# Performance work log

Measured on AMD Instinct MI355X. Metric: run time of the kernel, lower is better.

The kernel has to match this reference:

```python
import jax, jax.numpy as jnp
import numpy as np

N = 250000   # atoms
E = 500000   # directed bond edges
B = 10000    # molecules
IN = 39      # atom feature dim (in_channels)
H = 128      # hidden_channels
ED = 10      # edge_dim
NUM_TIMESTEPS = 2


def setup_inputs() -> dict:
    key = jax.random.key(0)
    ks = iter(jax.random.split(key, 40))
    p = lambda shape: jax.random.normal(next(ks), shape, dtype=jnp.float32) * 0.05
    inp = {}
    inp["x"] = jax.random.normal(next(ks), (N, IN), dtype=jnp.float32)
    inp["edge_attr"] = jax.random.normal(next(ks), (E, ED), dtype=jnp.float32)
    # lin1
    inp["W_lin1"] = p((H, IN)); inp["b_lin1"] = p((H,))
    # GATEConv
    inp["gate_W1"] = p((H, H + ED)); inp["gate_W2"] = p((H, H))
    inp["gate_att_l"] = p((H,)); inp["gate_att_r"] = p((H,)); inp["gate_bias"] = p((H,))
    # GRUCell after GATEConv
    inp["gru1_Wih"] = p((3 * H, H)); inp["gru1_Whh"] = p((3 * H, H))
    inp["gru1_bih"] = p((3 * H,)); inp["gru1_bhh"] = p((3 * H,))
    # atom GATConv (num_layers-1 == 1)
    inp["conv_W"] = p((H, H)); inp["conv_att_src"] = p((H,)); inp["conv_att_dst"] = p((H,)); inp["conv_bias"] = p((H,))
    inp["gru2_Wih"] = p((3 * H, H)); inp["gru2_Whh"] = p((3 * H, H))
    inp["gru2_bih"] = p((3 * H,)); inp["gru2_bhh"] = p((3 * H,))
    # mol GATConv (bipartite atoms -> molecules, shared lin)
    inp["mol_W"] = p((H, H)); inp["mol_att_src"] = p((H,)); inp["mol_att_dst"] = p((H,)); inp["mol_bias"] = p((H,))
    inp["grum_Wih"] = p((3 * H, H)); inp["grum_Whh"] = p((3 * H, H))
    inp["grum_bih"] = p((3 * H,)); inp["grum_bhh"] = p((3 * H,))
    # lin2 + head
    inp["W_lin2"] = p((H, H)); inp["b_lin2"] = p((H,))
    inp["W_head"] = p((1, H)); inp["b_head"] = p((1,))
    inp["edge_index"] = jax.random.randint(next(ks), (2, E), 0, N, dtype=jnp.int32)
    inp["batch"] = jnp.sort(jax.random.randint(next(ks), (N,), 0, B, dtype=jnp.int32))
    return inp


def _gru(xg, hg, Wih, Whh, bih, bhh):
    # torch.nn.GRUCell semantics
    gi = xg @ Wih.T + bih
    gh = hg @ Whh.T + bhh
    ir, iz, inn = jnp.split(gi, 3, axis=-1)
    hr, hz, hn = jnp.split(gh, 3, axis=-1)
    r = jax.nn.sigmoid(ir + hr)
    z = jax.nn.sigmoid(iz + hz)
    n = jnp.tanh(inn + r * hn)
    return (1.0 - z) * n + z * hg


def _seg_softmax(logits, seg, num):
    # PyG softmax over target-index segments (stable, +1e-16 denom)
    m = jax.ops.segment_max(logits, seg, num_segments=num)
    e = jnp.exp(logits - m[seg])
    s = jax.ops.segment_sum(e, seg, num_segments=num)
    return e / (s[seg] + 1e-16)


def reference(x, edge_attr, W_lin1, b_lin1, gate_W1, gate_W2, gate_att_l, gate_att_r, gate_bias,
              gru1_Wih, gru1_Whh, gru1_bih, gru1_bhh,
              conv_W, conv_att_src, conv_att_dst, conv_bias,
              gru2_Wih, gru2_Whh, gru2_bih, gru2_bhh,
              mol_W, mol_att_src, mol_att_dst, mol_bias,
              grum_Wih, grum_Whh, grum_bih, grum_bhh,
              W_lin2, b_lin2, W_head, b_head,
              edge_index, batch):
    lrelu = lambda v: jax.nn.leaky_relu(v, 0.01)
    src, dst = edge_index[0], edge_index[1]  # (j, i): messages flow j -> i
    # initial atom embedding
    x = lrelu(x @ W_lin1.T + b_lin1)
    # ---- GATEConv (edge-attr-aware attention, aggr='add') ----
    xj = x[src]                                                   # [E, H]
    he = lrelu(jnp.concatenate([xj, edge_attr], axis=-1) @ gate_W1.T)
    alpha = lrelu(he @ gate_att_l + x[dst] @ gate_att_r)          # [E]
    alpha = _seg_softmax(alpha, dst, N)
    h = jax.ops.segment_sum((xj @ gate_W2.T) * alpha[:, None], dst, num_segments=N) + gate_bias
    h = jax.nn.elu(h)
    x = jax.nn.relu(_gru(h, x, gru1_Wih, gru1_Whh, gru1_bih, gru1_bhh))
    # ---- atom GATConv (heads=1, neg_slope=0.01, no self loops) ----
    xl = x @ conv_W.T
    a = lrelu((xl * conv_att_src).sum(-1)[src] + (xl * conv_att_dst).sum(-1)[dst])
    a = _seg_softmax(a, dst, N)
    h = jax.ops.segment_sum(xl[src] * a[:, None], dst, num_segments=N) + conv_bias
    h = jax.nn.relu(h)
    x = jax.nn.relu(_gru(h, x, gru2_Wih, gru2_Whh, gru2_bih, gru2_bhh))
    # ---- attentive graph readout: bipartite GAT atoms -> molecules ----
    out = jax.nn.relu(jax.ops.segment_sum(x, batch, num_segments=B))  # [B, H]
    for _ in range(NUM_TIMESTEPS):
        xs = x @ mol_W.T                                          # src transform [N, H]
        od = out @ mol_W.T                                        # dst transform [B, H]
        a = lrelu((xs * mol_att_src).sum(-1) + ((od * mol_att_dst).sum(-1))[batch])
        a = _seg_softmax(a, batch, B)
        h = jax.ops.segment_sum(xs * a[:, None], batch, num_segments=B) + mol_bias
        h = jax.nn.elu(h)
        out = jax.nn.relu(_gru(h, out, grum_Wih, grum_Whh, grum_bih, grum_bhh))
    out = out @ W_lin2.T + b_lin2
    out = out @ W_head.T + b_head                                 # [B, 1]
    return out.squeeze(-1)                                        # [B]
```

## Files before the change

### kernel.cpp

```cpp
#include <hip/hip_runtime.h>
#include <hip/hip_bf16.h>
#include <type_traits>

typedef __hip_bfloat16 bf16;

constexpr int N_  = 250000;
constexpr int E_  = 500000;
constexpr int B_  = 10000;
constexpr int H_  = 128;

typedef short s8v __attribute__((ext_vector_type(8)));
typedef float f4v __attribute__((ext_vector_type(4)));

__device__ __forceinline__ float b2f(bf16 v){ return __bfloat162float(v); }
__device__ __forceinline__ bf16  f2b(float v){ return __float2bfloat16(v); }
__device__ __forceinline__ float lrelu_f(float v){ return v > 0.f ? v : 0.01f*v; }
__device__ __forceinline__ float sigmoid_f(float x){ return __builtin_amdgcn_rcpf(1.f+__expf(-x)); }
__device__ __forceinline__ float tanh_f(float x){ return 1.f - 2.f*__builtin_amdgcn_rcpf(__expf(2.f*x)+1.f); }
__device__ __forceinline__ float elu_f(float v){ return v > 0.f ? v : __expf(v)-1.f; }
__device__ __forceinline__ unsigned f2b_bits(float f){
  bf16 h=__float2bfloat16(f); unsigned short s; __builtin_memcpy(&s,&h,2); return (unsigned)s;
}
__device__ __forceinline__ void unp8(uint4 v, float* o){
  o[0]=__uint_as_float(v.x<<16); o[1]=__uint_as_float(v.x&0xffff0000u);
  o[2]=__uint_as_float(v.y<<16); o[3]=__uint_as_float(v.y&0xffff0000u);
  o[4]=__uint_as_float(v.z<<16); o[5]=__uint_as_float(v.z&0xffff0000u);
  o[6]=__uint_as_float(v.w<<16); o[7]=__uint_as_float(v.w&0xffff0000u);
}

struct W2B { const float* s; bf16* d; int rows, ld, ow, cw; };
struct W2B9 { W2B seg[9]; };
__global__ void w2ball_k(W2B9 p){
  W2B g=p.seg[blockIdx.y];
  int i=blockIdx.x*256+threadIdx.x;
  if (i>=g.rows*g.ow) return;
  int r=i/g.ow, k=i-r*g.ow;
  g.d[i] = f2b(k<g.cw ? g.s[(size_t)r*g.ld+k] : 0.f);
}

__global__ __launch_bounds__(256) void lin1_mfma_k(const float* __restrict__ X0, const bf16* __restrict__ Wb,
                            const float* __restrict__ bias, const float* __restrict__ dvec,
                            bf16* __restrict__ Y, float* __restrict__ dout, int M){
  __shared__ __align__(16) bf16 sx[64][72];
  __shared__ float sdot[4][64];
  int wv=threadIdx.x>>6, lane=threadIdx.x&63;
  int n=lane&15, q=lane>>4;
  int c0=wv*32;
  s8v wB[2][2];
  #pragma unroll
  for (int ct=0;ct<2;ct++)
    #pragma unroll
    for (int kk=0;kk<2;kk++)
      wB[ct][kk]=*(const s8v*)(Wb+(size_t)(c0+ct*16+n)*64+kk*32+q*8);
  float bb[2];
  #pragma unroll
  for (int ct=0;ct<2;ct++) bb[ct]=bias[c0+ct*16+n];
  float va[2]={dvec[c0+n], dvec[c0+16+n]};
  for (int i=threadIdx.x;i<64*25;i+=256){ int r=i/25,k=39+(i-(i/25)*25); sx[r][k]=f2b(0.f); }
  for (long r0=(long)blockIdx.x*64; r0<M; r0+=(long)gridDim.x*64){
    __syncthreads();
    for (int f=threadIdx.x; f<64*39; f+=256){
      int r=f/39, k=f-(f/39)*39; long row=r0+r;
      sx[r][k]= f2b(row<M ? X0[row*39+k] : 0.f);
    }
    __syncthreads();
    s8v a[4][2];
    #pragma unroll
    for (int rt=0;rt<4;rt++)
      #pragma unroll
      for (int kk=0;kk<2;kk++)
        a[rt][kk]=*(const s8v*)&sx[rt*16+n][kk*32+q*8];
    f4v acc[4][2];
    #pragma unroll
    for (int rt=0;rt<4;rt++)
      #pragma unroll
      for (int ct=0;ct<2;ct++) acc[rt][ct]=(f4v){0.f,0.f,0.f,0.f};
    #pragma unroll
    for (int kk=0;kk<2;kk++)
      #pragma unroll
      for (int rt=0;rt<4;rt++)
        #pragma unroll
        for (int ct=0;ct<2;ct++)
          acc[rt][ct]=__builtin_amdgcn_mfma_f32_16x16x32_bf16(a[rt][kk],wB[ct][kk],acc[rt][ct],0,0,0);
    #pragma unroll
    for (int rt=0;rt<4;rt++){
      #pragma unroll
      for (int rg=0;rg<4;rg++){
        float y0=lrelu_f(acc[rt][0][rg]+bb[0]);
        float y1=lrelu_f(acc[rt][1][rg]+bb[1]);
        long row=r0+rt*16+q*4+rg;
        if (row<M){
          Y[row*128+c0+n]   =f2b(y0);
          Y[row*128+c0+16+n]=f2b(y1);
        }
        float pa=y0*va[0]+y1*va[1];
        #pragma unroll
        for (int o=1;o<16;o<<=1) pa+=__shfl_xor(pa,o);
        if (n==0) sdot[wv][rt*16+q*4+rg]=pa;
      }
    }
    __syncthreads();
    if (threadIdx.x<64){
      long row=r0+threadIdx.x;
      if (row<M) dout[row]=sdot[0][threadIdx.x]+sdot[1][threadIdx.x]+sdot[2][threadIdx.x]+sdot[3][threadIdx.x];
    }
  }
}

template<int ACT,int NDOT>
__global__ __launch_bounds__(256) void lin_mfma_k(const bf16* __restrict__ X, const bf16* __restrict__ Wb,
                            const float* __restrict__ bias, bf16* __restrict__ Y,
                            const float* __restrict__ v1, const float* __restrict__ v2,
                            float* __restrict__ d1, float* __restrict__ d2, int M){
  __shared__ float sdot[2][4][64];
  int wv=threadIdx.x>>6, lane=threadIdx.x&63;
  int n=lane&15, q=lane>>4;
  int c0=wv*32;
  s8v wB[2][4];
  #pragma unroll
  for (int ct=0;ct<2;ct++)
    #pragma unroll
    for (int kk=0;kk<4;kk++)
      wB[ct][kk]=*(const s8v*)(Wb+(size_t)(c0+ct*16+n)*128+kk*32+q*8);
  float bb[2];
  #pragma unroll
  for (int ct=0;ct<2;ct++) bb[ct]=bias? bias[c0+ct*16+n]:0.f;
  float va[2][2];
  if constexpr (NDOT>=1){ va[0][0]=v1[c0+n]; va[0][1]=v1[c0+16+n]; }
  if constexpr (NDOT>=2){ va[1][0]=v2[c0+n]; va[1][1]=v2[c0+16+n]; }
  for (long r0=(long)blockIdx.x*64; r0<M; r0+=(long)gridDim.x*64){
    s8v a[4][4];
    #pragma unroll
    for (int rt=0;rt<4;rt++){
      long row=r0+rt*16+n; if (row>=M) row=M-1;
      #pragma unroll
      for (int kk=0;kk<4;kk++) a[rt][kk]=*(const s8v*)(X+row*128+kk*32+q*8);
    }
    f4v acc[4][2];
    #pragma unroll
    for (int rt=0;rt<4;rt++)
      #pragma unroll
      for (int ct=0;ct<2;ct++) acc[rt][ct]=(f4v){0.f,0.f,0.f,0.f};
    #pragma unroll
    for (int kk=0;kk<4;kk++)
      #pragma unroll
      for (int rt=0;rt<4;rt++)
        #pragma unroll
        for (int ct=0;ct<2;ct++)
          acc[rt][ct]=__builtin_amdgcn_mfma_f32_16x16x32_bf16(a[rt][kk],wB[ct][kk],acc[rt][ct],0,0,0);
    #pragma unroll
    for (int rt=0;rt<4;rt++){
      #pragma unroll
      for (int rg=0;rg<4;rg++){
        float y0=acc[rt][0][rg]+bb[0];
        float y1=acc[rt][1][rg]+bb[1];
        if (ACT==2){ y0=elu_f(y0); y1=elu_f(y1); }
        long row=r0+rt*16+q*4+rg;
        if (row<M){
          Y[row*128+c0+n]   =f2b(y0);
          Y[row*128+c0+16+n]=f2b(y1);
        }
        if constexpr (NDOT>=1){
          float pa=y0*va[0][0]+y1*va[0][1];
          float pb=0.f;
          if constexpr (NDOT>=2) pb=y0*va[1][0]+y1*va[1][1];
          #pragma unroll
          for (int o=1;o<16;o<<=1){
            pa+=__shfl_xor(pa,o);
            if constexpr (NDOT>=2) pb+=__shfl_xor(pb,o);
          }
          if (n==0){
            sdot[0][wv][rt*16+q*4+rg]=pa;
            if constexpr (NDOT>=2) sdot[1][wv][rt*16+q*4+rg]=pb;
          }
        }
      }
    }
    if constexpr (NDOT>=1){
      __syncthreads();
      if (threadIdx.x<64){
        long row=r0+threadIdx.x;
        if (row<M){
          d1[row]=sdot[0][0][threadIdx.x]+sdot[0][1][threadIdx.x]+sdot[0][2][threadIdx.x]+sdot[0][3][threadIdx.x];
          if constexpr (NDOT>=2)
            d2[row]=sdot[1][0][threadIdx.x]+sdot[1][1][threadIdx.x]+sdot[1][2][threadIdx.x]+sdot[1][3][threadIdx.x];
        }
      }
      __syncthreads();
    }
  }
}

__global__ __launch_bounds__(512,1) void gru_mfma_k(const bf16* __restrict__ A, const bf16* __restrict__ X,
                            const bf16* __restrict__ Wih, const bf16* __restrict__ Whh,
                            const float* __restrict__ bih, const float* __restrict__ bhh,
                            bf16* __restrict__ dest, int M){
  __shared__ __align__(16) bf16 sA[2][32][136];
  __shared__ __align__(16) bf16 sX[2][32][136];
  int wv=threadIdx.x>>6, lane=threadIdx.x&63;
  int n=lane&15, q=lane>>4;
  int c0=wv*16;
  s8v wI[3][4], wH[3][4];
  #pragma unroll
  for (int g=0;g<3;g++)
    #pragma unroll
    for (int kk=0;kk<4;kk++){
      size_t off=((size_t)(g*128+c0+n))*128+kk*32+q*8;
      wI[g][kk]=*(const s8v*)(Wih+off);
      wH[g][kk]=*(const s8v*)(Whh+off);
    }
  int col=c0+n;
  float br =bih[col]+bhh[col];
  float bz =bih[128+col]+bhh[128+col];
  float bni=bih[256+col], bnh=bhh[256+col];

  int srow=wv*4+q;
  int schunk=n;
  long step=(long)gridDim.x*32;
  long r0=(long)blockIdx.x*32;
  int buf=0;
  {
    long rowg=r0+srow; if (rowg>=M) rowg=M-1;
    uint4 va=*(const uint4*)(A+rowg*128+schunk*8);
    uint4 vx=*(const uint4*)(X+rowg*128+schunk*8);
    *(uint4*)&sA[0][srow][schunk*8]=va;
    *(uint4*)&sX[0][srow][schunk*8]=vx;
  }
  __syncthreads();
  for (; r0<M; r0+=step){
    long rn=r0+step;
    uint4 va, vx; bool pre = rn<M;
    if (pre){
      long rowg=rn+srow; if (rowg>=M) rowg=M-1;
      va=*(const uint4*)(A+rowg*128+schunk*8);
      vx=*(const uint4*)(X+rowg*128+schunk*8);
    }
    f4v acc[6][2];
    #pragma unroll
    for (int g=0;g<6;g++)
      #pragma unroll
      for (int rt=0;rt<2;rt++) acc[g][rt]=(f4v){0.f,0.f,0.f,0.f};
    #pragma unroll
    for (int kk=0;kk<4;kk++){
      s8v aA[2], aX[2];
      #pragma unroll
      for (int rt=0;rt<2;rt++){
        aA[rt]=*(const s8v*)&sA[buf][rt*16+n][(kk*4+q)*8];
        aX[rt]=*(const s8v*)&sX[buf][rt*16+n][(kk*4+q)*8];
      }
      #pragma unroll
      for (int g=0;g<3;g++)
        #pragma unroll
        for (int rt=0;rt<2;rt++){
          acc[g  ][rt]=__builtin_amdgcn_mfma_f32_16x16x32_bf16(aA[rt],wI[g][kk],acc[g  ][rt],0,0,0);
          acc[3+g][rt]=__builtin_amdgcn_mfma_f32_16x16x32_bf16(aX[rt],wH[g][kk],acc[3+g][rt],0,0,0);
        }
    }
    float xv[2][4];
    #pragma unroll
    for (int rt=0;rt<2;rt++)
      #pragma unroll
      for (int rg=0;rg<4;rg++)
        xv[rt][rg]=b2f(sX[buf][rt*16+q*4+rg][col]);
    #pragma unroll
    for (int rt=0;rt<2;rt++){
      #pragma unroll
      for (int rg=0;rg<4;rg++){
        long row=r0+rt*16+q*4+rg;
        if (row<M){
          float rgate=sigmoid_f(acc[0][rt][rg]+acc[3][rt][rg]+br);
          float zgate=sigmoid_f(acc[1][rt][rg]+acc[4][rt][rg]+bz);
          float nn=tanh_f(acc[2][rt][rg]+bni + rgate*(acc[5][rt][rg]+bnh));
          float o=(1.f-zgate)*nn + zgate*xv[rt][rg];
          dest[row*128+col]=f2b(fmaxf(o,0.f));
        }
      }
    }
    if (pre){
      *(uint4*)&sA[buf^1][srow][schunk*8]=va;
      *(uint4*)&sX[buf^1][srow][schunk*8]=vx;
    }
    __syncthreads();
    buf^=1;
  }
}

__global__ __launch_bounds__(256) void gru_scalar_k(const float* __restrict__ A, const float* __restrict__ X,
                            const float* __restrict__ Wih, const float* __restrict__ Whh,
                            const float* __restrict__ bih, const float* __restrict__ bhh,
                            float* __restrict__ dest, int M){
  __shared__ unsigned sW[6][32*66];
  __shared__ float sA[8][132], sX[8][132];
  __shared__ float sbi[3][32], sbh[3][32];
  int c0 = blockIdx.y*32;
  for (int i=threadIdx.x; i<6*32*64; i+=256){
    int m=i>>11, r=i&2047, c=r>>6, k2=r&63;
    const float* base = (m<3)? Wih : Whh;
    int g = (m<3)? m : m-3;
    const float* wp = base + ((size_t)(g*128 + c0 + c))*128 + 2*k2;
    sW[m][c*66 + k2] = f2b_bits(wp[0]) | (f2b_bits(wp[1])<<16);
  }
  if (threadIdx.x < 96){
    int g=threadIdx.x>>5, c=threadIdx.x&31;
    sbi[g][c]=bih[g*128+c0+c]; sbh[g][c]=bhh[g*128+c0+c];
  }
  __syncthreads();
  int sub=threadIdx.x>>5, c=threadIdx.x&31;
  for (long r0=(long)blockIdx.x*8; r0<M; r0+=(long)gridDim.x*8){
    __syncthreads();
    for (int i=threadIdx.x;i<8*16;i+=256){
      int rr=i>>4, q=i&15; long row=r0+rr;
      if (row<M){
        *(float4*)&sA[rr][q*8]   = *(const float4*)(A+row*128+q*8);
        *(float4*)&sA[rr][q*8+4] = *(const float4*)(A+row*128+q*8+4);
        *(float4*)&sX[rr][q*8]   = *(const float4*)(X+row*128+q*8);
        *(float4*)&sX[rr][q*8+4] = *(const float4*)(X+row*128+q*8+4);
      } else {
        float4 z=make_float4(0,0,0,0);
        *(float4*)&sA[rr][q*8]=z; *(float4*)&sA[rr][q*8+4]=z;
        *(float4*)&sX[rr][q*8]=z; *(float4*)&sX[rr][q*8+4]=z;
      }
    }
    __syncthreads();
    long row=r0+sub;
    if (row<M){
      const unsigned* wri=&sW[0][c*66]; const unsigned* wzi=&sW[1][c*66]; const unsigned* wni=&sW[2][c*66];
      const unsigned* wrh=&sW[3][c*66]; const unsigned* wzh=&sW[4][c*66]; const unsigned* wnh=&sW[5][c*66];
      const float2* xa=(const float2*)sA[sub]; const float2* xb=(const float2*)sX[sub];
      float ari=0,azi=0,ani=0,arh=0,azh=0,anh=0;
      #pragma unroll 8
      for (int k2=0;k2<64;k2++){
        float2 av=xa[k2], bv=xb[k2];
        unsigned u;
        u=wri[k2]; ari += av.x*__uint_as_float(u<<16) + av.y*__uint_as_float(u&0xffff0000u);
        u=wzi[k2]; azi += av.x*__uint_as_float(u<<16) + av.y*__uint_as_float(u&0xffff0000u);
        u=wni[k2]; ani += av.x*__uint_as_float(u<<16) + av.y*__uint_as_float(u&0xffff0000u);
        u=wrh[k2]; arh += bv.x*__uint_as_float(u<<16) + bv.y*__uint_as_float(u&0xffff0000u);
        u=wzh[k2]; azh += bv.x*__uint_as_float(u<<16) + bv.y*__uint_as_float(u&0xffff0000u);
        u=wnh[k2]; anh += bv.x*__uint_as_float(u<<16) + bv.y*__uint_as_float(u&0xffff0000u);
      }
      float rg = sigmoid_f(ari+arh+sbi[0][c]+sbh[0][c]);
      float zg = sigmoid_f(azi+azh+sbi[1][c]+sbh[1][c]);
      float nn = tanh_f(ani+sbi[2][c] + rg*(anh+sbh[2][c]));
      float xv = sX[sub][c0+c];
      float o  = (1.f-zg)*nn + zg*xv;
      dest[row*128+c0+c] = fmaxf(o,0.f);
    }
  }
}

__global__ __launch_bounds__(256) void gate_edge_logits_k(const bf16* __restrict__ u, const float* __restrict__ ea,
                                   const float* __restrict__ gW1, const float* __restrict__ att_l,
                                   const float* __restrict__ ddst, const int* __restrict__ src,
                                   const int* __restrict__ dst, const int* __restrict__ epos,
                                   float* __restrict__ elog, int E){
  int wv=threadIdx.x>>6, lane=threadIdx.x&63;
  int t=lane&31;
  float w[10][4];
  #pragma unroll
  for (int k=0;k<10;k++)
    #pragma unroll
    for (int j=0;j<4;j++)
      w[k][j]=gW1[(size_t)(t*4+j)*138 + 128 + k];
  float al[4];
  #pragma unroll
  for (int j=0;j<4;j++) al[j]=att_l[t*4+j];

  long stride=(long)gridDim.x*8;
  long e=(long)blockIdx.x*8 + wv*2 + (lane>>5);
  if (e>=E) return;
  int sj=src[e];
  uint2 uv=*(const uint2*)(u+(size_t)sj*128+t*4);
  const float2* er=(const float2*)(ea+(size_t)e*10);
  float2 c0=er[0],c1=er[1],c2=er[2],c3=er[3],c4=er[4];
  float dv=ddst[dst[e]];
  int ep=epos[e];
  while (true){
    long en=e+stride; bool has=en<E;
    uint2 uvn=make_uint2(0,0);
    float2 d0={0,0},d1={0,0},d2={0,0},d3={0,0},d4={0,0};
    float dvn=0.f; int epn=0;
    if (has){
      int sjn=src[en];
      uvn=*(const uint2*)(u+(size_t)sjn*128+t*4);
      const float2* ern=(const float2*)(ea+(size_t)en*10);
      d0=ern[0];d1=ern[1];d2=ern[2];d3=ern[3];d4=ern[4];
      dvn=ddst[dst[en]];
      epn=epos[en];
    }
    float uf[4];
    uf[0]=__uint_as_float(uv.x<<16); uf[1]=__uint_as_float(uv.x&0xffff0000u);
    uf[2]=__uint_as_float(uv.y<<16); uf[3]=__uint_as_float(uv.y&0xffff0000u);
    float acc=0.f;
    #pragma unroll
    for (int j=0;j<4;j++){
      float v=uf[j];
      v+=c0.x*w[0][j]; v+=c0.y*w[1][j];
      v+=c1.x*w[2][j]; v+=c1.y*w[3][j];
      v+=c2.x*w[4][j]; v+=c2.y*w[5][j];
      v+=c3.x*w[6][j]; v+=c3.y*w[7][j];
      v+=c4.x*w[8][j]; v+=c4.y*w[9][j];
      acc+=lrelu_f(v)*al[j];
    }
    #pragma unroll
    for (int o=16;o;o>>=1) acc+=__shfl_xor(acc,o);
    if (t==0) elog[ep]=lrelu_f(acc+dv);
    if (!has) break;
    e=en; uv=uvn; c0=d0;c1=d1;c2=d2;c3=d3;c4=d4; dv=dvn; ep=epn;
  }
}

template<int ACT>
__global__ void node_gather_k(const float* __restrict__ elog, const int* __restrict__ srcp,
                              const int* __restrict__ ptr, const bf16* __restrict__ V,
                              const float* __restrict__ bias, bf16* __restrict__ S, int M){
  int wv=threadIdx.x>>6, lane=threadIdx.x&63;
  int g=lane>>3, t=lane&7;
  int node=blockIdx.x*32 + wv*8 + g;
  if (node>=M) return;
  int p0=ptr[node], p1=ptr[node+1];
  float m=-INFINITY;
  for (int p=p0+t;p<p1;p+=8) m=fmaxf(m,elog[p]);
  #pragma unroll
  for (int o=4;o;o>>=1) m=fmaxf(m,__shfl_xor(m,o));
  float ssum=0.f;
  float acc[16]={0,0,0,0,0,0,0,0,0,0,0,0,0,0,0,0};
  if (p0<p1){
    float lg=elog[p0];
    const uint4* vp=(const uint4*)(V+(size_t)srcp[p0]*128+t*16);
    uint4 va=vp[0], vb=vp[1];
    for (int p=p0+1;p<p1;p++){
      float lgn=elog[p];
      const uint4* vpn=(const uint4*)(V+(size_t)srcp[p]*128+t*16);
      uint4 van=vpn[0], vbn=vpn[1];
      float e=__expf(lg-m); ssum+=e;
      float xf[8]; unp8(va,xf);
      #pragma unroll
      for (int j=0;j<8;j++) acc[j]+=e*xf[j];
      unp8(vb,xf);
      #pragma unroll
      for (int j=0;j<8;j++) acc[8+j]+=e*xf[j];
      lg=lgn; va=van; vb=vbn;
    }
    float e=__expf(lg-m); ssum+=e;
    float xf[8]; unp8(va,xf);
    #pragma unroll
    for (int j=0;j<8;j++) acc[j]+=e*xf[j];
    unp8(vb,xf);
    #pragma unroll
    for (int j=0;j<8;j++) acc[8+j]+=e*xf[j];
  }
  float inv=1.f/(ssum+1e-16f);
  #pragma unroll
  for (int j=0;j<16;j++) acc[j]*=inv;
  if (ACT==1){
    #pragma unroll
    for (int j=0;j<16;j++) acc[j]=fmaxf(acc[j]+bias[t*16+j],0.f);
  }
  uint4 o1,o2;
  o1.x=f2b_bits(acc[0])|(f2b_bits(acc[1])<<16);
  o1.y=f2b_bits(acc[2])|(f2b_bits(acc[3])<<16);
  o1.z=f2b_bits(acc[4])|(f2b_bits(acc[5])<<16);
  o1.w=f2b_bits(acc[6])|(f2b_bits(acc[7])<<16);
  o2.x=f2b_bits(acc[8])|(f2b_bits(acc[9])<<16);
  o2.y=f2b_bits(acc[10])|(f2b_bits(acc[11])<<16);
  o2.z=f2b_bits(acc[12])|(f2b_bits(acc[13])<<16);
  o2.w=f2b_bits(acc[14])|(f2b_bits(acc[15])<<16);
  *(uint4*)(S+(size_t)node*128+t*16)=o1;
  *(uint4*)(S+(size_t)node*128+t*16+8)=o2;
}

__global__ __launch_bounds__(256) void conv_gather_k(const float* __restrict__ dsrc, const float* __restrict__ ddst,
    const int* __restrict__ ptr, const int* __restrict__ srcp,
    const bf16* __restrict__ V, const float* __restrict__ bias, bf16* __restrict__ S, int M){
  int wv=threadIdx.x>>6, lane=threadIdx.x&63;
  int g=lane>>3, t=lane&7;
  int node=blockIdx.x*32 + wv*8 + g;
  if (node>=M) return;
  int p0=ptr[node], p1=ptr[node+1];
  float dvn=ddst[node];
  float m=-INFINITY, s=0.f;
  float acc[16]={0,0,0,0,0,0,0,0,0,0,0,0,0,0,0,0};
  if (p0<p1){
    int sj=srcp[p0];
    float ls=dsrc[sj];
    const uint4* vp=(const uint4*)(V+(size_t)sj*128+t*16);
    uint4 va=vp[0], vb=vp[1];
    for (int p=p0+1;p<p1;p++){
      int sjn=srcp[p];
      float lsn=dsrc[sjn];
      const uint4* vpn=(const uint4*)(V+(size_t)sjn*128+t*16);
      uint4 van=vpn[0], vbn=vpn[1];
      float l=lrelu_f(ls+dvn);
      float mn=fmaxf(m,l), sc=__expf(m-mn), ee=__expf(l-mn);
      float xf[8]; unp8(va,xf);
      s=s*sc+ee;
      #pragma unroll
      for (int j=0;j<8;j++) acc[j]=acc[j]*sc+ee*xf[j];
      unp8(vb,xf);
      #pragma unroll
      for (int j=0;j<8;j++) acc[8+j]=acc[8+j]*sc+ee*xf[j];
      m=mn; ls=lsn; va=van; vb=vbn;
    }
    float l=lrelu_f(ls+dvn);
    float mn=fmaxf(m,l), sc=__expf(m-mn), ee=__expf(l-mn);
    float xf[8]; unp8(va,xf);
    s=s*sc+ee;
    #pragma unroll
    for (int j=0;j<8;j++) acc[j]=acc[j]*sc+ee*xf[j];
    unp8(vb,xf);
    #pragma unroll
    for (int j=0;j<8;j++) acc[8+j]=acc[8+j]*sc+ee*xf[j];
  }
  float inv=1.f/(s+1e-16f);
  float r[16];
  #pragma unroll
  for (int j=0;j<16;j++) r[j]=fmaxf(acc[j]*inv+bias[t*16+j],0.f);
  uint4 o1,o2;
  o1.x=f2b_bits(r[0])|(f2b_bits(r[1])<<16);
  o1.y=f2b_bits(r[2])|(f2b_bits(r[3])<<16);
  o1.z=f2b_bits(r[4])|(f2b_bits(r[5])<<16);
  o1.w=f2b_bits(r[6])|(f2b_bits(r[7])<<16);
  o2.x=f2b_bits(r[8])|(f2b_bits(r[9])<<16);
  o2.y=f2b_bits(r[10])|(f2b_bits(r[11])<<16);
  o2.z=f2b_bits(r[12])|(f2b_bits(r[13])<<16);
  o2.w=f2b_bits(r[14])|(f2b_bits(r[15])<<16);
  *(uint4*)(S+(size_t)node*128+t*16)=o1;
  *(uint4*)(S+(size_t)node*128+t*16+8)=o2;
}

__global__ void mol_ptr_k(const int* __restrict__ batch, int* __restrict__ mptr, int n, int Bn){
  int b=blockIdx.x*256+threadIdx.x; if (b>Bn) return;
  if (b==Bn){ mptr[Bn]=n; return; }
  int lo=0, hi=n;
  while (lo<hi){ int mid=(lo+hi)>>1; if (batch[mid]<b) lo=mid+1; else hi=mid; }
  mptr[b]=lo;
}

__global__ void mol_sum_k(const bf16* __restrict__ x, const int* __restrict__ mptr,
                          float* __restrict__ out, int Bn){
  int wv=threadIdx.x>>6, lane=threadIdx.x&63;
  int b=blockIdx.x*4+wv; if (b>=Bn) return;
  int p0=mptr[b], p1=mptr[b+1];
  float a0=0.f,a1=0.f;
  for (int i=p0;i<p1;i++){ a0+=b2f(x[(size_t)i*128+lane]); a1+=b2f(x[(size_t)i*128+64+lane]); }
  out[(size_t)b*128+lane]=fmaxf(a0,0.f); out[(size_t)b*128+64+lane]=fmaxf(a1,0.f);
}

__global__ void fold_att_k(const float* __restrict__ W, const float* __restrict__ att,
                           float* __restrict__ wdd){
  int k=threadIdx.x; float a=0.f;
  for (int c=0;c<128;c++) a+=att[c]*W[(size_t)c*128+k];
  wdd[k]=a;
}

__global__ __launch_bounds__(256) void mol_fused_k(const float* __restrict__ dsrc, const int* __restrict__ mptr,
    const bf16* __restrict__ xs, const float* __restrict__ wdd, const float* __restrict__ outc,
    const float* __restrict__ bias, float* __restrict__ hb, int Bn){
  int wv=threadIdx.x>>6, lane=threadIdx.x&63;
  long b=(long)blockIdx.x*4+wv; if (b>=Bn) return;
  int p0=mptr[b], p1=mptr[b+1];
  float dd=outc[(size_t)b*128+lane]*wdd[lane]+outc[(size_t)b*128+64+lane]*wdd[64+lane];
  #pragma unroll
  for (int o=32;o;o>>=1) dd+=__shfl_xor(dd,o);
  float m=-INFINITY, s=0.f, a0=0.f, a1=0.f;
  for (int i=p0;i<p1;i++){
    float a=lrelu_f(dsrc[i]+dd);
    float x0=b2f(xs[(size_t)i*128+lane]), x1=b2f(xs[(size_t)i*128+64+lane]);
    float mn=fmaxf(m,a), sc=__expf(m-mn), ee=__expf(a-mn);
    s=s*sc+ee; a0=a0*sc+ee*x0; a1=a1*sc+ee*x1; m=mn;
  }
  float inv=1.f/(s+1e-16f);
  hb[(size_t)b*128+lane]=elu_f(a0*inv+bias[lane]);
  hb[(size_t)b*128+64+lane]=elu_f(a1*inv+bias[64+lane]);
}

__global__ void fold_head_k(const float* __restrict__ W2, const float* __restrict__ b2,
                            const float* __restrict__ Wh, const float* __restrict__ bh,
                            float* __restrict__ v){
  __shared__ float sred[128];
  int k=threadIdx.x;
  float a=0.f;
  for (int c=0;c<128;c++) a+=Wh[c]*W2[(size_t)c*128+k];
  v[k]=a;
  sred[k]=b2[k]*Wh[k]; __syncthreads();
  for (int o=64;o;o>>=1){ if (k<o) sred[k]+=sred[k+o]; __syncthreads(); }
  if (k==0) v[128]=sred[0]+bh[0];
}

__global__ void head_dot_k(const float* __restrict__ out, const float* __restrict__ v,
                           float* __restrict__ y, int M){
  __shared__ float sv[129];
  if (threadIdx.x<129) sv[threadIdx.x]=v[threadIdx.x];
  __syncthreads();
  int wv=threadIdx.x>>6, lane=threadIdx.x&63;
  long row=(long)blockIdx.x*4+wv;
  if (row>=M) return;
  float a=out[row*128+lane]*sv[lane]+out[row*128+64+lane]*sv[64+lane];
  #pragma unroll
  for (int o=32;o;o>>=1) a+=__shfl_xor(a,o);
  if (!lane) y[row]=a+sv[128];
}

__global__ void zero_i32_k(int* p, int n){ int i=blockIdx.x*256+threadIdx.x; if (i<n) p[i]=0; }
__global__ void hist_k(const int* __restrict__ dst, int* __restrict__ deg, int n){
  int e=blockIdx.x*256+threadIdx.x; if (e<n) atomicAdd(&deg[dst[e]],1);
}
__global__ void scan1_k(const int* __restrict__ deg, int* __restrict__ ptr,
                        int* __restrict__ part, int n){
  __shared__ int sd[256];
  int base=blockIdx.x*1024, tid=threadIdx.x;
  int v[4]; int ssum=0;
  #pragma unroll
  for (int j=0;j<4;j++){ int idx=base+tid*4+j; v[j]= idx<n? deg[idx]:0; ssum+=v[j]; }
  sd[tid]=ssum; __syncthreads();
  for (int o=1;o<256;o<<=1){ int t = tid>=o? sd[tid-o]:0; __syncthreads(); sd[tid]+=t; __syncthreads(); }
  int excl=sd[tid]-ssum;
  #pragma unroll
  for (int j=0;j<4;j++){ int idx=base+tid*4+j; if (idx<n) ptr[idx]=excl; excl+=v[j]; }
  if (tid==255) part[blockIdx.x]=sd[255];
}
__global__ void scan2_k(int* part, int nb){
  __shared__ int sd[512];
  int tid=threadIdx.x;
  int v= tid<nb? part[tid]:0; sd[tid]=v; __syncthreads();
  for (int o=1;o<512;o<<=1){ int t = tid>=o? sd[tid-o]:0; __syncthreads(); sd[tid]+=t; __syncthreads(); }
  if (tid<nb) part[tid]=sd[tid]-v;
}
__global__ void scan3_k(int* __restrict__ ptr, const int* __restrict__ part,
                        int* __restrict__ wofs, int n, int total){
  int i=blockIdx.x*256+threadIdx.x;
  if (i<n){ int val=ptr[i]+part[i>>10]; ptr[i]=val; wofs[i]=val; }
  if (i==0) ptr[n]=total;
}
__global__ void fill_csr_k(const int* __restrict__ dst, const int* __restrict__ src,
                           int* __restrict__ wofs, int* __restrict__ srcp,
                           int* __restrict__ epos, int n){
  int e=blockIdx.x*256+threadIdx.x;
  if (e<n){ int p=atomicAdd(&wofs[dst[e]],1); srcp[p]=src[e]; epos[e]=p; }
}

extern "C" void kernel_launch(void* const* d_in, const int* in_sizes, int n_in,
                              void* d_out, int out_size, void* d_ws, size_t ws_size,
                              hipStream_t stream){
  (void)in_sizes; (void)n_in; (void)out_size; (void)ws_size;
  const float* x0        =(const float*)d_in[0];
  const float* edge_attr =(const float*)d_in[1];
  const float* W_lin1    =(const float*)d_in[2];
  const float* b_lin1    =(const float*)d_in[3];
  const float* gate_W1   =(const float*)d_in[4];
  const float* gate_W2   =(const float*)d_in[5];
  const float* gate_att_l=(const float*)d_in[6];
  const float* gate_att_r=(const float*)d_in[7];
  const float* gate_bias =(const float*)d_in[8];
  const float* g1_Wih=(const float*)d_in[9];  const float* g1_Whh=(const float*)d_in[10];
  const float* g1_bih=(const float*)d_in[11]; const float* g1_bhh=(const float*)d_in[12];
  const float* conv_W=(const float*)d_in[13];
  const float* conv_att_src=(const float*)d_in[14];
  const float* conv_att_dst=(const float*)d_in[15];
  const float* conv_bias   =(const float*)d_in[16];
  const float* g2_Wih=(const float*)d_in[17]; const float* g2_Whh=(const float*)d_in[18];
  const float* g2_bih=(const float*)d_in[19]; const float* g2_bhh=(const float*)d_in[20];
  const float* mol_W=(const float*)d_in[21];
  const float* mol_att_src=(const float*)d_in[22];
  const float* mol_att_dst=(const float*)d_in[23];
  const float* mol_bias   =(const float*)d_in[24];
  const float* gm_Wih=(const float*)d_in[25]; const float* gm_Whh=(const float*)d_in[26];
  const float* gm_bih=(const float*)d_in[27]; const float* gm_bhh=(const float*)d_in[28];
  const float* W_lin2=(const float*)d_in[29]; const float* b_lin2=(const float*)d_in[30];
  const float* W_head=(const float*)d_in[31]; const float* b_head=(const float*)d_in[32];
  const int* ei   =(const int*)d_in[33];
  const int* batch=(const int*)d_in[34];
  const int* src=ei; const int* dst=ei+E_;
  float* y=(float*)d_out;

  const size_t NH=(size_t)N_*H_, BH=(size_t)B_*H_;
  bf16* b0  =(bf16*)d_ws;
  bf16* b1  =b0+NH;
  bf16* b2v =b1+NH;
  float* outA=(float*)(b2v+NH);
  float* outB=outA+BH;
  float* hb  =outB+BH;
  float* elog=hb+BH;
  float* dsrc=elog+E_;
  float* ddst=dsrc+N_;
  float* alog=ddst+N_;
  float* wdd =alog+N_;
  float* dd  =wdd+128;
  int* deg =(int*)(dd+B_);
  int* ptr =deg+N_;
  int* wofs=ptr+N_+1;
  int* part=wofs+N_;
  int* mptr=part+512;
  int* srcp=mptr+B_+1;
  int* epos=srcp+E_;
  uintptr_t wbase=((uintptr_t)(epos+E_)+255)&~(uintptr_t)255;
  bf16* wb_gw1 =(bf16*)wbase;
  bf16* wb_gw2 =wb_gw1 +128*128;
  bf16* wb_conv=wb_gw2 +128*128;
  bf16* wb_mol =wb_conv+128*128;
  bf16* wb_g1i =wb_mol +128*128;
  bf16* wb_g1h =wb_g1i +384*128;
  bf16* wb_g2i =wb_g1h +384*128;
  bf16* wb_g2h =wb_g2i +384*128;
  bf16* wb_l1  =wb_g2h +384*128;

  W2B9 wp;
  wp.seg[0]={gate_W1,wb_gw1,128,138,128,128};
  wp.seg[1]={gate_W2,wb_gw2,128,128,128,128};
  wp.seg[2]={conv_W ,wb_conv,128,128,128,128};
  wp.seg[3]={mol_W  ,wb_mol ,128,128,128,128};
  wp.seg[4]={g1_Wih,wb_g1i,384,128,128,128};
  wp.seg[5]={g1_Whh,wb_g1h,384,128,128,128};
  wp.seg[6]={g2_Wih,wb_g2i,384,128,128,128};
  wp.seg[7]={g2_Whh,wb_g2h,384,128,128,128};
  wp.seg[8]={W_lin1,wb_l1 ,128, 39, 64, 39};
  w2ball_k<<<dim3(192,9),256,0,stream>>>(wp);

  zero_i32_k<<<(N_+255)/256,256,0,stream>>>(deg,N_);
  hist_k<<<(E_+255)/256,256,0,stream>>>(dst,deg,E_);
  int nb=(N_+1023)/1024;
  scan1_k<<<nb,256,0,stream>>>(deg,ptr,part,N_);
  scan2_k<<<1,512,0,stream>>>(part,nb);
  scan3_k<<<(N_+255)/256,256,0,stream>>>(ptr,part,wofs,N_,E_);
  fill_csr_k<<<(E_+255)/256,256,0,stream>>>(dst,src,wofs,srcp,epos,E_);
  mol_ptr_k<<<(B_+1+255)/256,256,0,stream>>>(batch,mptr,N_,B_);

  lin1_mfma_k<<<1024,256,0,stream>>>(x0,wb_l1,b_lin1,gate_att_r,b0,ddst,N_);

  const int GL=768, GN8=(N_+31)/32;
  lin_mfma_k<0,0><<<GL,256,0,stream>>>(b0,wb_gw1,nullptr,b1,nullptr,nullptr,nullptr,nullptr,N_);
  gate_edge_logits_k<<<8192,256,0,stream>>>(b1,edge_attr,gate_W1,gate_att_l,ddst,src,dst,epos,elog,E_);
  node_gather_k<0><<<GN8,256,0,stream>>>(elog,srcp,ptr,b0,nullptr,b2v,N_);
  lin_mfma_k<2,0><<<GL,256,0,stream>>>(b2v,wb_gw2,gate_bias,b1,nullptr,nullptr,nullptr,nullptr,N_);
  gru_mfma_k<<<1024,512,0,stream>>>(b1,b0,wb_g1i,wb_g1h,g1_bih,g1_bhh,b2v,N_);
  lin_mfma_k<0,2><<<GL,256,0,stream>>>(b2v,wb_conv,nullptr,b0,conv_att_src,conv_att_dst,dsrc,ddst,N_);
  conv_gather_k<<<GN8,256,0,stream>>>(dsrc,ddst,ptr,srcp,b0,conv_bias,b1,N_);
  gru_mfma_k<<<1024,512,0,stream>>>(b1,b2v,wb_g2i,wb_g2h,g2_bih,g2_bhh,b0,N_);
  mol_sum_k<<<(B_+3)/4,256,0,stream>>>(b0,mptr,outA,B_);
  lin_mfma_k<0,1><<<GL,256,0,stream>>>(b0,wb_mol,nullptr,b1,mol_att_src,nullptr,dsrc,nullptr,N_);
  fold_att_k<<<1,128,0,stream>>>(mol_W,mol_att_dst,wdd);
  float* out_cur=outA; float* out_nxt=outB;
  dim3 gm(157,4);
  for (int ts=0; ts<2; ts++){
    mol_fused_k<<<(B_+3)/4,256,0,stream>>>(dsrc,mptr,b1,wdd,out_cur,mol_bias,hb,B_);
    gru_scalar_k<<<gm,256,0,stream>>>(hb,out_cur,gm_Wih,gm_Whh,gm_bih,gm_bhh,out_nxt,B_);
    float* tmp=out_cur; out_cur=out_nxt; out_nxt=tmp;
  }
  fold_head_k<<<1,128,0,stream>>>(W_lin2,b_lin2,W_head,b_head,elog);
  head_dot_k<<<(B_+3)/4,256,0,stream>>>(out_cur,elog,y,B_);
}
```

Measured before the change: 1.068 ms.

## Fuse gate W1 projection into lin1 and gate W2 projection into node gather

The lin1 kernel now stages its bf16 output tile in shared memory and immediately runs the gate W1 MFMA projection, writing both outputs. This removes a separate linear pass over N×128. The node softmax-gather kernel now stages its aggregated rows in shared memory and applies the gate W2 projection with bias and ELU in place, replacing another full linear kernel and its round-trip through global memory. The price is more registers and shared memory per block, plus an extra __syncthreads in the gather kernel.

New measurement: 1.090 ms. 2.0% more time.

```diff
diff --git a/kernel.cpp b/kernel.cpp
--- a/kernel.cpp
+++ b/kernel.cpp
@@ -38,10 +38,13 @@
   g.d[i] = f2b(k<g.cw ? g.s[(size_t)r*g.ld+k] : 0.f);
 }
 
-__global__ __launch_bounds__(256) void lin1_mfma_k(const float* __restrict__ X0, const bf16* __restrict__ Wb,
+__global__ __launch_bounds__(256) void lin1_gw1_k(const float* __restrict__ X0, const bf16* __restrict__ Wb,
                             const float* __restrict__ bias, const float* __restrict__ dvec,
-                            bf16* __restrict__ Y, float* __restrict__ dout, int M){
+                            const bf16* __restrict__ Wg,
+                            bf16* __restrict__ Y, bf16* __restrict__ U,
+                            float* __restrict__ dout, int M){
   __shared__ __align__(16) bf16 sx[64][72];
+  __shared__ __align__(16) bf16 sy[64][136];
   __shared__ float sdot[4][64];
   int wv=threadIdx.x>>6, lane=threadIdx.x&63;
   int n=lane&15, q=lane>>4;
@@ -52,6 +55,12 @@
     #pragma unroll
     for (int kk=0;kk<2;kk++)
       wB[ct][kk]=*(const s8v*)(Wb+(size_t)(c0+ct*16+n)*64+kk*32+q*8);
+  s8v wG[2][4];
+  #pragma unroll
+  for (int ct=0;ct<2;ct++)
+    #pragma unroll
+    for (int kk=0;kk<4;kk++)
+      wG[ct][kk]=*(const s8v*)(Wg+(size_t)(c0+ct*16+n)*128+kk*32+q*8);
   float bb[2];
   #pragma unroll
   for (int ct=0;ct<2;ct++) bb[ct]=bias[c0+ct*16+n];
@@ -88,21 +97,53 @@
       for (int rg=0;rg<4;rg++){
         float y0=lrelu_f(acc[rt][0][rg]+bb[0]);
         float y1=lrelu_f(acc[rt][1][rg]+bb[1]);
-        long row=r0+rt*16+q*4+rg;
+        int lr=rt*16+q*4+rg;
+        long row=r0+lr;
+        bf16 h0=f2b(y0), h1=f2b(y1);
+        sy[lr][c0+n]   =h0;
+        sy[lr][c0+16+n]=h1;
         if (row<M){
-          Y[row*128+c0+n]   =f2b(y0);
-          Y[row*128+c0+16+n]=f2b(y1);
+          Y[row*128+c0+n]   =h0;
+          Y[row*128+c0+16+n]=h1;
         }
         float pa=y0*va[0]+y1*va[1];
         #pragma unroll
         for (int o=1;o<16;o<<=1) pa+=__shfl_xor(pa,o);
-        if (n==0) sdot[wv][rt*16+q*4+rg]=pa;
+        if (n==0) sdot[wv][lr]=pa;
       }
     }
     __syncthreads();
     if (threadIdx.x<64){
       long row=r0+threadIdx.x;
       if (row<M) dout[row]=sdot[0][threadIdx.x]+sdot[1][threadIdx.x]+sdot[2][threadIdx.x]+sdot[3][threadIdx.x];
+    }
+    f4v acc2[4][2];
+    #pragma unroll
+    for (int rt=0;rt<4;rt++)
+      #pragma unroll
+      for (int ct=0;ct<2;ct++) acc2[rt][ct]=(f4v){0.f,0.f,0.f,0.f};
+    #pragma unroll
+    for (int kk=0;kk<4;kk++){
+      s8v a2[4];
+      #pragma unroll
+      for (int rt=0;rt<4;rt++) a2[rt]=*(const s8v*)&sy[rt*16+n][kk*32+q*8];
+      #pragma unroll
+      for (int rt=0;rt<4;rt++)
+        #pragma unroll
+        for (int ct=0;ct<2;ct++)
+          acc2[rt][ct]=__builtin_amdgcn_mfma_f32_16x16x32_bf16(a2[rt],wG[ct][kk],acc2[rt][ct],0,0,0);
+    }
+    #pragma unroll
+    for (int ct=0;ct<2;ct++){
+      int col=c0+ct*16+n;
+      #pragma unroll
+      for (int rt=0;rt<4;rt++){
+        #pragma unroll
+        for (int rg=0;rg<4;rg++){
+          long row=r0+rt*16+q*4+rg;
+          if (row<M) U[row*128+col]=f2b(acc2[rt][ct][rg]);
+        }
+      }
     }
   }
 }
@@ -410,29 +451,48 @@
   }
 }
 
-template<int ACT>
-__global__ void node_gather_k(const float* __restrict__ elog, const int* __restrict__ srcp,
+__global__ __launch_bounds__(256) void node_gather_gw2_k(const float* __restrict__ elog, const int* __restrict__ srcp,
                               const int* __restrict__ ptr, const bf16* __restrict__ V,
-                              const float* __restrict__ bias, bf16* __restrict__ S, int M){
+                              const bf16* __restrict__ Wg, const float* __restrict__ gbias,
+                              bf16* __restrict__ Hout, int M){
+  __shared__ __align__(16) bf16 sS[32][136];
   int wv=threadIdx.x>>6, lane=threadIdx.x&63;
   int g=lane>>3, t=lane&7;
-  int node=blockIdx.x*32 + wv*8 + g;
-  if (node>=M) return;
-  int p0=ptr[node], p1=ptr[node+1];
-  float m=-INFINITY;
-  for (int p=p0+t;p<p1;p+=8) m=fmaxf(m,elog[p]);
-  #pragma unroll
-  for (int o=4;o;o>>=1) m=fmaxf(m,__shfl_xor(m,o));
+  int base=blockIdx.x*32;
+  int node=base + wv*8 + g;
+  int n=lane&15, q=lane>>4;
+  int c0=wv*32;
+  s8v wG[2][4];
+  #pragma unroll
+  for (int ct=0;ct<2;ct++)
+    #pragma unroll
+    for (int kk=0;kk<4;kk++)
+      wG[ct][kk]=*(const s8v*)(Wg+(size_t)(c0+ct*16+n)*128+kk*32+q*8);
   float ssum=0.f;
   float acc[16]={0,0,0,0,0,0,0,0,0,0,0,0,0,0,0,0};
-  if (p0<p1){
-    float lg=elog[p0];
-    const uint4* vp=(const uint4*)(V+(size_t)srcp[p0]*128+t*16);
-    uint4 va=vp[0], vb=vp[1];
-    for (int p=p0+1;p<p1;p++){
-      float lgn=elog[p];
-      const uint4* vpn=(const uint4*)(V+(size_t)srcp[p]*128+t*16);
-      uint4 van=vpn[0], vbn=vpn[1];
+  if (node<M){
+    int p0=ptr[node], p1=ptr[node+1];
+    float m=-INFINITY;
+    for (int p=p0+t;p<p1;p+=8) m=fmaxf(m,elog[p]);
+    #pragma unroll
+    for (int o=4;o;o>>=1) m=fmaxf(m,__shfl_xor(m,o));
+    if (p0<p1){
+      float lg=elog[p0];
+      const uint4* vp=(const uint4*)(V+(size_t)srcp[p0]*128+t*16);
+      uint4 va=vp[0], vb=vp[1];
+      for (int p=p0+1;p<p1;p++){
+        float lgn=elog[p];
+        const uint4* vpn=(const uint4*)(V+(size_t)srcp[p]*128+t*16);
+        uint4 van=vpn[0], vbn=vpn[1];
+        float e=__expf(lg-m); ssum+=e;
+        float xf[8]; unp8(va,xf);
+        #pragma unroll
+        for (int j=0;j<8;j++) acc[j]+=e*xf[j];
+        unp8(vb,xf);
+        #pragma unroll
+        for (int j=0;j<8;j++) acc[8+j]+=e*xf[j];
+        lg=lgn; va=van; vb=vbn;
+      }
       float e=__expf(lg-m); ssum+=e;
       float xf[8]; unp8(va,xf);
       #pragma unroll
@@ -440,23 +500,11 @@
       unp8(vb,xf);
       #pragma unroll
       for (int j=0;j<8;j++) acc[8+j]+=e*xf[j];
-      lg=lgn; va=van; vb=vbn;
-    }
-    float e=__expf(lg-m); ssum+=e;
-    float xf[8]; unp8(va,xf);
-    #pragma unroll
-    for (int j=0;j<8;j++) acc[j]+=e*xf[j];
-    unp8(vb,xf);
-    #pragma unroll
-    for (int j=0;j<8;j++) acc[8+j]+=e*xf[j];
+    }
   }
   float inv=1.f/(ssum+1e-16f);
   #pragma unroll
   for (int j=0;j<16;j++) acc[j]*=inv;
-  if (ACT==1){
-    #pragma unroll
-    for (int j=0;j<16;j++) acc[j]=fmaxf(acc[j]+bias[t*16+j],0.f);
-  }
   uint4 o1,o2;
   o1.x=f2b_bits(acc[0])|(f2b_bits(acc[1])<<16);
   o1.y=f2b_bits(acc[2])|(f2b_bits(acc[3])<<16);
@@ -466,8 +514,39 @@
   o2.y=f2b_bits(acc[10])|(f2b_bits(acc[11])<<16);
   o2.z=f2b_bits(acc[12])|(f2b_bits(acc[13])<<16);
   o2.w=f2b_bits(acc[14])|(f2b_bits(acc[15])<<16);
-  *(uint4*)(S+(size_t)node*128+t*16)=o1;
-  *(uint4*)(S+(size_t)node*128+t*16+8)=o2;
+  int r=wv*8+g;
+  *(uint4*)&sS[r][t*16]  =o1;
+  *(uint4*)&sS[r][t*16+8]=o2;
+  __syncthreads();
+  f4v acc2[2][2];
+  #pragma unroll
+  for (int rt=0;rt<2;rt++)
+    #pragma unroll
+    for (int ct=0;ct<2;ct++) acc2[rt][ct]=(f4v){0.f,0.f,0.f,0.f};
+  #pragma unroll
+  for (int kk=0;kk<4;kk++){
+    s8v aS[2];
+    #pragma unroll
+    for (int rt=0;rt<2;rt++) aS[rt]=*(const s8v*)&sS[rt*16+n][kk*32+q*8];
+    #pragma unroll
+    for (int rt=0;rt<2;rt++)
+      #pragma unroll
+      for (int ct=0;ct<2;ct++)
+        acc2[rt][ct]=__builtin_amdgcn_mfma_f32_16x16x32_bf16(aS[rt],wG[ct][kk],acc2[rt][ct],0,0,0);
+  }
+  #pragma unroll
+  for (int ct=0;ct<2;ct++){
+    int col=c0+ct*16+n;
+    float bcol=gbias[col];
+    #pragma unroll
+    for (int rt=0;rt<2;rt++){
+      #pragma unroll
+      for (int rg=0;rg<4;rg++){
+        long row=base+rt*16+q*4+rg;
+        if (row<M) Hout[row*128+col]=f2b(elu_f(acc2[rt][ct][rg]+bcol));
+      }
+    }
+  }
 }
 
 __global__ __launch_bounds__(256) void conv_gather_k(const float* __restrict__ dsrc, const float* __restrict__ ddst,
@@ -726,16 +805,14 @@
   fill_csr_k<<<(E_+255)/256,256,0,stream>>>(dst,src,wofs,srcp,epos,E_);
   mol_ptr_k<<<(B_+1+255)/256,256,0,stream>>>(batch,mptr,N_,B_);
 
-  lin1_mfma_k<<<1024,256,0,stream>>>(x0,wb_l1,b_lin1,gate_att_r,b0,ddst,N_);
-
-  const int GL=768, GN8=(N_+31)/32;
-  lin_mfma_k<0,0><<<GL,256,0,stream>>>(b0,wb_gw1,nullptr,b1,nullptr,nullptr,nullptr,nullptr,N_);
+  lin1_gw1_k<<<1024,256,0,stream>>>(x0,wb_l1,b_lin1,gate_att_r,wb_gw1,b0,b1,ddst,N_);
+
+  const int GL=768, GN32=(N_+31)/32;
   gate_edge_logits_k<<<8192,256,0,stream>>>(b1,edge_attr,gate_W1,gate_att_l,ddst,src,dst,epos,elog,E_);
-  node_gather_k<0><<<GN8,256,0,stream>>>(elog,srcp,ptr,b0,nullptr,b2v,N_);
-  lin_mfma_k<2,0><<<GL,256,0,stream>>>(b2v,wb_gw2,gate_bias,b1,nullptr,nullptr,nullptr,nullptr,N_);
+  node_gather_gw2_k<<<GN32,256,0,stream>>>(elog,srcp,ptr,b0,wb_gw2,gate_bias,b1,N_);
   gru_mfma_k<<<1024,512,0,stream>>>(b1,b0,wb_g1i,wb_g1h,g1_bih,g1_bhh,b2v,N_);
   lin_mfma_k<0,2><<<GL,256,0,stream>>>(b2v,wb_conv,nullptr,b0,conv_att_src,conv_att_dst,dsrc,ddst,N_);
-  conv_gather_k<<<GN8,256,0,stream>>>(dsrc,ddst,ptr,srcp,b0,conv_bias,b1,N_);
+  conv_gather_k<<<GN32,256,0,stream>>>(dsrc,ddst,ptr,srcp,b0,conv_bias,b1,N_);
   gru_mfma_k<<<1024,512,0,stream>>>(b1,b2v,wb_g2i,wb_g2h,g2_bih,g2_bhh,b0,N_);
   mol_sum_k<<<(B_+3)/4,256,0,stream>>>(b0,mptr,outA,B_);
   lin_mfma_k<0,1><<<GL,256,0,stream>>>(b0,wb_mol,nullptr,b1,mol_att_src,nullptr,dsrc,nullptr,N_);
```
